# Optimization experiments

Hardware: AMD Instinct MI355X
Metric: run time of the kernel (lower is better)

The kernel has to match this reference:

```python
import jax, jax.numpy as jnp
import numpy as np

# Dims: B batch, T target seq, S source seq (self-attn: S==T), V symmetry-rep dim (D4 -> 8),
# M heads-per-group, K groups (num_heads = M*K = 8), F head_rep dim (TrivialRep -> 1),
# Hqk qk head width, Hv v head width, C feature width per rep component.
B, T, S, V, M, K, F, Hqk, Hv, C = 4, 512, 512, 8, 2, 4, 1, 32, 32, 256


def setup_inputs() -> dict:
    key = jax.random.key(0)
    ks = jax.random.split(key, 6)
    x = jax.random.normal(ks[0], (B, T, V, C), jnp.float32)
    # SymDecompLinear kernels: q has extra out reps (F, M, K); k/v have (F, 1, K) -> m axis broadcast
    Wq = jax.random.normal(ks[1], (C, M, K, F, Hqk), jnp.float32) / np.sqrt(C).astype(np.float32)
    Wk = jax.random.normal(ks[2], (C, K, F, Hqk), jnp.float32) / np.sqrt(C).astype(np.float32)
    Wv = jax.random.normal(ks[3], (C, K, F, Hv), jnp.float32) / np.sqrt(C).astype(np.float32)
    # out projection contracts the (M, K, F, Hv) head structure back to C features
    Wout = jax.random.normal(ks[4], (M, K, F, Hv, C), jnp.float32) / np.sqrt(M * K * F * Hv).astype(np.float32)
    mask = jax.random.bernoulli(ks[5], 0.9, (B, T, S))
    mask = mask.at[..., 0].set(True)  # guarantee each query attends to >=1 key
    return dict(x=x, Wq=Wq, Wk=Wk, Wv=Wv, Wout=Wout, mask=mask)


def reference(x, Wq, Wk, Wv, Wout, mask):
    # projections: q -> [B,T,V,M,K,F,Hqk]; k,v -> [B,S,V,K,F,H] (single head per group, broadcast over m)
    q = jnp.einsum('btvc,cmkfh->btvmkfh', x, Wq)
    k = jnp.einsum('bsvc,ckfh->bsvkfh', x, Wk)
    v = jnp.einsum('bsvc,ckfh->bsvkfh', x, Wv)
    scale = 1.0 / np.sqrt(F * Hqk).astype(np.float32)
    # logits retain the symmetry axis v: [B,T,S,V,M,K]
    logits = scale * jnp.einsum('btvmkfh,bsvkfh->btsvmk', q, k)
    lgmsk = mask[..., :, :, None, None, None]  # [B,T,S,1,1,1]
    weight = jax.nn.softmax(logits, axis=-4, where=lgmsk)  # softmax over source axis s
    att = jnp.einsum('btsvmk,bsvkfh->btvmkfh', weight, v)
    out = jnp.einsum('btvmkfh,mkfhc->btvc', att, Wout)
    return out
```

## Files before the change

kernel.cpp:

```cpp
#include <hip/hip_runtime.h>
#include <hip/hip_bf16.h>
#include <cstdint>

#define BB 4
#define TT 512
#define SS 512
#define VV 8
#define NROWS (BB * TT * VV)

typedef __attribute__((ext_vector_type(8))) short bf16x8;
typedef __attribute__((ext_vector_type(4))) float f32x4;

static __device__ __forceinline__ short f2bf(float f) {
  union { float f; unsigned u; } x; x.f = f;
  unsigned r = x.u + 0x7FFFu + ((x.u >> 16) & 1u);
  return (short)(r >> 16);
}

__global__ __launch_bounds__(256) void pack_w_kernel(const float* __restrict__ Wq,
                                                     const float* __restrict__ Wk,
                                                     const float* __restrict__ Wv,
                                                     const float* __restrict__ Wout,
                                                     short* __restrict__ WcatT,
                                                     short* __restrict__ WoutT) {
  int idx = blockIdx.x * 256 + threadIdx.x;
  const float qscale = 0.17677669529663687f * 1.4426950408889634f;
  if (idx < 512 * 256) {
    int n = idx >> 8, c = idx & 255;
    float val;
    if (n < 256)      val = Wq[c * 256 + n] * qscale;
    else if (n < 384) val = Wk[c * 128 + (n - 256)];
    else              val = Wv[c * 128 + (n - 384)];
    WcatT[idx] = f2bf(val);
  } else {
    int j = idx - 512 * 256;
    int cc = j >> 8, jj = j & 255;
    WoutT[j] = f2bf(Wout[jj * 256 + cc]);
  }
}

__global__ __launch_bounds__(256) void pack_mask_kernel(const int* __restrict__ mask,
                                                        unsigned long long* __restrict__ mask64) {
  int row = blockIdx.x * 4 + (threadIdx.x >> 6);
  int ln = threadIdx.x & 63;
  const int* mrow = mask + (size_t)row * SS;
#pragma unroll
  for (int c = 0; c < 8; ++c) {
    unsigned long long bal = __ballot(mrow[c * 64 + ln] != 0);
    if (ln == 0) mask64[(size_t)row * 8 + c] = bal;
  }
}

template <int N, bool AF32, bool OUTF32>
__global__ __launch_bounds__(256) void gemm_bf16(const void* __restrict__ Ap,
                                                 const short* __restrict__ Bt,
                                                 void* __restrict__ Cout) {
  __shared__ short As[128][64];
  __shared__ short Bs[128][64];
  const int tid = threadIdx.x;
  const int w = tid >> 6, ln = tid & 63;
  const int wr = (w >> 1) * 64, wc = (w & 1) * 64;
  const int bm = blockIdx.x * 128, bn = blockIdx.y * 128;
  const int lr = ln & 15, lk = (ln >> 4) * 8;
  const int r0 = tid >> 3, ko = (tid & 7) * 8;

  f32x4 acc[4][4] = {};

  for (int k0 = 0; k0 < 256; k0 += 64) {
    bf16x8 a[4], bb[4];
#pragma unroll
    for (int i = 0; i < 4; ++i) {
      size_t row = (size_t)(bm + i * 32 + r0);
      if constexpr (AF32) {
        const float* Af = (const float*)Ap;
        float4 f0 = *(const float4*)&Af[row * 256 + k0 + ko];
        float4 f1 = *(const float4*)&Af[row * 256 + k0 + ko + 4];
        bf16x8 o;
        o[0]=f2bf(f0.x); o[1]=f2bf(f0.y); o[2]=f2bf(f0.z); o[3]=f2bf(f0.w);
        o[4]=f2bf(f1.x); o[5]=f2bf(f1.y); o[6]=f2bf(f1.z); o[7]=f2bf(f1.w);
        a[i] = o;
      } else {
        a[i] = *(const bf16x8*)&((const short*)Ap)[row * 256 + k0 + ko];
      }
      bb[i] = *(const bf16x8*)&Bt[(size_t)(bn + i * 32 + r0) * 256 + k0 + ko];
    }
    __syncthreads();
#pragma unroll
    for (int i = 0; i < 4; ++i) {
      *(bf16x8*)&As[i * 32 + r0][ko] = a[i];
      *(bf16x8*)&Bs[i * 32 + r0][ko] = bb[i];
    }
    __syncthreads();

#pragma unroll
    for (int kk = 0; kk < 2; ++kk) {
      bf16x8 af[4], bfr[4];
#pragma unroll
      for (int mi = 0; mi < 4; ++mi)
        af[mi] = *(const bf16x8*)&As[wr + mi * 16 + lr][kk * 32 + lk];
#pragma unroll
      for (int ni = 0; ni < 4; ++ni)
        bfr[ni] = *(const bf16x8*)&Bs[wc + ni * 16 + lr][kk * 32 + lk];
#pragma unroll
      for (int mi = 0; mi < 4; ++mi)
#pragma unroll
        for (int ni = 0; ni < 4; ++ni)
          acc[mi][ni] = __builtin_amdgcn_mfma_f32_16x16x32_bf16(af[mi], bfr[ni], acc[mi][ni], 0, 0, 0);
    }
  }

  const int rowg = (ln >> 4) * 4;
#pragma unroll
  for (int mi = 0; mi < 4; ++mi)
#pragma unroll
    for (int r = 0; r < 4; ++r) {
      size_t row = bm + wr + mi * 16 + rowg + r;
#pragma unroll
      for (int ni = 0; ni < 4; ++ni) {
        int col = bn + wc + ni * 16 + lr;
        if (OUTF32) ((float*)Cout)[row * N + col] = acc[mi][ni][r];
        else        ((short*)Cout)[row * N + col] = f2bf(acc[mi][ni][r]);
      }
    }
}

__global__ __launch_bounds__(512) void attn_mfma(const short* __restrict__ qkv,
                                                 const unsigned long long* __restrict__ mask64,
                                                 short* __restrict__ att) {
  const int t0 = blockIdx.x * 128;
  const int v  = blockIdx.y >> 2;
  const int k  = blockIdx.y & 3;
  const int b  = blockIdx.z;
  const int tid = threadIdx.x;
  const int w  = tid >> 6;
  const int ln = tid & 63;
  const int gq = ln >> 4;
  const int tr = ln & 15;

  __shared__ short Kt[4][64][40];
  __shared__ short Vt[4][32][72];
  __shared__ short Pt[8][16][72];

  bf16x8 qf[2];
  {
    const short* qp = qkv + ((size_t)((b*TT + t0 + w*16 + tr)*VV + v))*512 + k*32 + gq*8;
    qf[0] = *(const bf16x8*)qp;
    qf[1] = *(const bf16x8*)(qp + 128);
  }

  f32x4 acc_o[2][2] = {};
  float m_run[2] = {-1e30f, -1e30f};
  float l_run[2] = {0.f, 0.f};

  const int sp  = tid >> 8;
  const int st2 = tid & 255;
  const int srow = st2 >> 2;
  const int hg = (st2 & 3) * 8;
  const unsigned long long* mrow = mask64 + ((size_t)(b*TT + t0 + w*16 + tr)) * 8;

  const short* src0 = qkv + ((size_t)((b*TT + sp*64 + srow)*VV + v))*512 + 256 + k*32 + hg;
  bf16x8 kreg = *(const bf16x8*)src0;
  bf16x8 vreg = *(const bf16x8*)(src0 + 128);

  for (int c2 = 0; c2 < 4; ++c2) {
    const int bufb = (c2 & 1) * 2;
    *(bf16x8*)&Kt[bufb + sp][srow][hg] = kreg;
#pragma unroll
    for (int j = 0; j < 8; ++j) Vt[bufb + sp][hg + j][srow] = vreg[j];
    __syncthreads();
    if (c2 < 3) {
      const short* src = qkv + ((size_t)((b*TT + (c2 + 1)*128 + sp*64 + srow)*VV + v))*512 + 256 + k*32 + hg;
      kreg = *(const bf16x8*)src;
      vreg = *(const bf16x8*)(src + 128);
    }

#pragma unroll
    for (int p = 0; p < 2; ++p) {
      unsigned long long mb = mrow[2 * c2 + p];
      unsigned mlo = (unsigned)mb, mhi = (unsigned)(mb >> 32);
      float bias[4][4];
#pragma unroll
      for (int st = 0; st < 4; ++st) {
        unsigned wbits = (st < 2) ? mlo : mhi;
        const int base = (st & 1) * 16 + 4 * gq;
#pragma unroll
        for (int r = 0; r < 4; ++r)
          bias[st][r] = ((wbits >> (base + r)) & 1u) ? 0.f : -INFINITY;
      }

      bf16x8 kf[4], vf[2][2];
#pragma unroll
      for (int st = 0; st < 4; ++st) kf[st] = *(const bf16x8*)&Kt[bufb + p][st*16 + tr][gq*8];
#pragma unroll
      for (int sh = 0; sh < 2; ++sh)
#pragma unroll
        for (int hh = 0; hh < 2; ++hh)
          vf[sh][hh] = *(const bf16x8*)&Vt[bufb + p][hh*16 + tr][sh*32 + gq*8];

#pragma unroll
      for (int m = 0; m < 2; ++m) {
        f32x4 lac[4];
#pragma unroll
        for (int st = 0; st < 4; ++st) {
          f32x4 z = {0.f, 0.f, 0.f, 0.f};
          lac[st] = __builtin_amdgcn_mfma_f32_16x16x32_bf16(kf[st], qf[m], z, 0, 0, 0);
        }
        float pl[4][4];
#pragma unroll
        for (int st = 0; st < 4; ++st)
#pragma unroll
          for (int r = 0; r < 4; ++r)
            pl[st][r] = lac[st][r] + bias[st][r];

        float cm = -INFINITY;
#pragma unroll
        for (int st = 0; st < 4; ++st)
#pragma unroll
          for (int r = 0; r < 4; ++r) cm = fmaxf(cm, pl[st][r]);
        cm = fmaxf(cm, __shfl_xor(cm, 16));
        cm = fmaxf(cm, __shfl_xor(cm, 32));

        bool skip = __all(cm - m_run[m] <= 11.5f);
        float mnew, corr;
        if (skip) { mnew = m_run[m]; corr = 1.f; }
        else {
          mnew = fmaxf(m_run[m], cm);
          corr = exp2f(m_run[m] - mnew);
          m_run[m] = mnew;
        }

        float rs = 0.f;
#pragma unroll
        for (int st = 0; st < 4; ++st)
#pragma unroll
          for (int r = 0; r < 4; ++r) {
            pl[st][r] = exp2f(pl[st][r] - mnew);
            rs += pl[st][r];
          }
        rs += __shfl_xor(rs, 16);
        rs += __shfl_xor(rs, 32);
        l_run[m] = l_run[m] * corr + rs;

        if (!skip) {
          float corrR[4];
#pragma unroll
          for (int r = 0; r < 4; ++r) corrR[r] = __shfl(corr, 4 * gq + r);
#pragma unroll
          for (int hh = 0; hh < 2; ++hh)
#pragma unroll
            for (int r = 0; r < 4; ++r) acc_o[m][hh][r] *= corrR[r];
        }

#pragma unroll
        for (int st = 0; st < 4; ++st) {
          unsigned d0 = ((unsigned)(unsigned short)f2bf(pl[st][1]) << 16) |
                        (unsigned)(unsigned short)f2bf(pl[st][0]);
          unsigned d1 = ((unsigned)(unsigned short)f2bf(pl[st][3]) << 16) |
                        (unsigned)(unsigned short)f2bf(pl[st][2]);
          *(uint2*)&Pt[w][tr][st * 16 + 4 * gq] = make_uint2(d0, d1);
        }
#pragma unroll
        for (int sh = 0; sh < 2; ++sh) {
          bf16x8 pf = *(const bf16x8*)&Pt[w][tr][sh * 32 + gq * 8];
#pragma unroll
          for (int hh = 0; hh < 2; ++hh)
            acc_o[m][hh] = __builtin_amdgcn_mfma_f32_16x16x32_bf16(pf, vf[sh][hh], acc_o[m][hh], 0, 0, 0);
        }
      }
    }
  }

#pragma unroll
  for (int m = 0; m < 2; ++m) {
    float invR[4];
#pragma unroll
    for (int r = 0; r < 4; ++r) invR[r] = 1.f / __shfl(l_run[m], 4 * gq + r);
#pragma unroll
    for (int r = 0; r < 4; ++r) {
      short* dst = att + ((size_t)((b*TT + t0 + w*16 + 4*gq + r)*VV + v))*256
                 + m*128 + k*32 + tr;
      dst[0]  = f2bf(acc_o[m][0][r] * invR[r]);
      dst[16] = f2bf(acc_o[m][1][r] * invR[r]);
    }
  }
}

extern "C" void kernel_launch(void* const* d_in, const int* in_sizes, int n_in,
                              void* d_out, int out_size, void* d_ws, size_t ws_size,
                              hipStream_t stream) {
  const float* x = (const float*)d_in[0];
  const float* Wq = (const float*)d_in[1];
  const float* Wk = (const float*)d_in[2];
  const float* Wv = (const float*)d_in[3];
  const float* Wout = (const float*)d_in[4];
  const int* mask = (const int*)d_in[5];
  float* out = (float*)d_out;

  short* WcatT = (short*)d_ws;
  short* WoutT = WcatT + 512 * 256;
  short* qkv   = WoutT + 256 * 256;
  short* att   = qkv + (size_t)NROWS * 512;
  unsigned long long* mask64 = (unsigned long long*)(att + (size_t)NROWS * 256);

  pack_w_kernel<<<(512 * 256 + 256 * 256) / 256, 256, 0, stream>>>(Wq, Wk, Wv, Wout, WcatT, WoutT);
  pack_mask_kernel<<<BB * TT / 4, 256, 0, stream>>>(mask, mask64);
  gemm_bf16<512, true, false><<<dim3(NROWS / 128, 4), 256, 0, stream>>>(x, WcatT, qkv);
  attn_mfma<<<dim3(TT / 128, VV * 4, BB), 512, 0, stream>>>(qkv, mask64, att);
  gemm_bf16<256, false, true><<<dim3(NROWS / 128, 2), 256, 0, stream>>>(att, WoutT, out);
}
```

Measured before the change: 81.33 us.

## Halve attention block size and use hardware packed bf16 conversion

New measurement: 72.08 us. 1.13x faster.

```diff
diff --git a/kernel.cpp b/kernel.cpp
--- a/kernel.cpp
+++ b/kernel.cpp
@@ -15,6 +15,12 @@
   union { float f; unsigned u; } x; x.f = f;
   unsigned r = x.u + 0x7FFFu + ((x.u >> 16) & 1u);
   return (short)(r >> 16);
+}
+
+static __device__ __forceinline__ unsigned cvt_pk(float lo, float hi) {
+  unsigned r;
+  asm("v_cvt_pk_bf16_f32 %0, %1, %2" : "=v"(r) : "v"(lo), "v"(hi));
+  return r;
 }
 
 __global__ __launch_bounds__(256) void pack_w_kernel(const float* __restrict__ Wq,
@@ -75,10 +81,9 @@
         const float* Af = (const float*)Ap;
         float4 f0 = *(const float4*)&Af[row * 256 + k0 + ko];
         float4 f1 = *(const float4*)&Af[row * 256 + k0 + ko + 4];
-        bf16x8 o;
-        o[0]=f2bf(f0.x); o[1]=f2bf(f0.y); o[2]=f2bf(f0.z); o[3]=f2bf(f0.w);
-        o[4]=f2bf(f1.x); o[5]=f2bf(f1.y); o[6]=f2bf(f1.z); o[7]=f2bf(f1.w);
-        a[i] = o;
+        uint4 pk = make_uint4(cvt_pk(f0.x, f0.y), cvt_pk(f0.z, f0.w),
+                              cvt_pk(f1.x, f1.y), cvt_pk(f1.z, f1.w));
+        a[i] = *(bf16x8*)&pk;
       } else {
         a[i] = *(const bf16x8*)&((const short*)Ap)[row * 256 + k0 + ko];
       }
@@ -115,19 +120,26 @@
 #pragma unroll
     for (int r = 0; r < 4; ++r) {
       size_t row = bm + wr + mi * 16 + rowg + r;
-#pragma unroll
-      for (int ni = 0; ni < 4; ++ni) {
-        int col = bn + wc + ni * 16 + lr;
-        if (OUTF32) ((float*)Cout)[row * N + col] = acc[mi][ni][r];
-        else        ((short*)Cout)[row * N + col] = f2bf(acc[mi][ni][r]);
-      }
-    }
-}
-
-__global__ __launch_bounds__(512) void attn_mfma(const short* __restrict__ qkv,
+      if constexpr (OUTF32) {
+#pragma unroll
+        for (int ni = 0; ni < 4; ++ni)
+          ((float*)Cout)[row * N + bn + wc + ni * 16 + lr] = acc[mi][ni][r];
+      } else {
+        unsigned u0 = cvt_pk(acc[mi][0][r], acc[mi][1][r]);
+        unsigned u1 = cvt_pk(acc[mi][2][r], acc[mi][3][r]);
+        short* Cs = (short*)Cout + row * N + bn + wc + lr;
+        Cs[0]  = (short)u0;
+        Cs[16] = (short)(u0 >> 16);
+        Cs[32] = (short)u1;
+        Cs[48] = (short)(u1 >> 16);
+      }
+    }
+}
+
+__global__ __launch_bounds__(256) void attn_mfma(const short* __restrict__ qkv,
                                                  const unsigned long long* __restrict__ mask64,
                                                  short* __restrict__ att) {
-  const int t0 = blockIdx.x * 128;
+  const int t0 = blockIdx.x * 64;
   const int v  = blockIdx.y >> 2;
   const int k  = blockIdx.y & 3;
   const int b  = blockIdx.z;
@@ -137,9 +149,9 @@
   const int gq = ln >> 4;
   const int tr = ln & 15;
 
-  __shared__ short Kt[4][64][40];
-  __shared__ short Vt[4][32][72];
-  __shared__ short Pt[8][16][72];
+  __shared__ short Kt[2][64][40];
+  __shared__ short Vt[2][32][72];
+  __shared__ short Pt[4][16][72];
 
   bf16x8 qf[2];
   {
@@ -152,120 +164,110 @@
   float m_run[2] = {-1e30f, -1e30f};
   float l_run[2] = {0.f, 0.f};
 
-  const int sp  = tid >> 8;
-  const int st2 = tid & 255;
-  const int srow = st2 >> 2;
-  const int hg = (st2 & 3) * 8;
+  const int srow = tid >> 2;
+  const int hg = (tid & 3) * 8;
   const unsigned long long* mrow = mask64 + ((size_t)(b*TT + t0 + w*16 + tr)) * 8;
 
-  const short* src0 = qkv + ((size_t)((b*TT + sp*64 + srow)*VV + v))*512 + 256 + k*32 + hg;
+  const short* src0 = qkv + ((size_t)((b*TT + srow)*VV + v))*512 + 256 + k*32 + hg;
   bf16x8 kreg = *(const bf16x8*)src0;
   bf16x8 vreg = *(const bf16x8*)(src0 + 128);
 
-  for (int c2 = 0; c2 < 4; ++c2) {
-    const int bufb = (c2 & 1) * 2;
-    *(bf16x8*)&Kt[bufb + sp][srow][hg] = kreg;
-#pragma unroll
-    for (int j = 0; j < 8; ++j) Vt[bufb + sp][hg + j][srow] = vreg[j];
+  for (int c = 0; c < 8; ++c) {
+    const int cur = c & 1;
+    *(bf16x8*)&Kt[cur][srow][hg] = kreg;
+#pragma unroll
+    for (int j = 0; j < 8; ++j) Vt[cur][hg + j][srow] = vreg[j];
     __syncthreads();
-    if (c2 < 3) {
-      const short* src = qkv + ((size_t)((b*TT + (c2 + 1)*128 + sp*64 + srow)*VV + v))*512 + 256 + k*32 + hg;
+    if (c < 7) {
+      const short* src = qkv + ((size_t)((b*TT + (c + 1) * 64 + srow)*VV + v))*512 + 256 + k*32 + hg;
       kreg = *(const bf16x8*)src;
       vreg = *(const bf16x8*)(src + 128);
     }
-
-#pragma unroll
-    for (int p = 0; p < 2; ++p) {
-      unsigned long long mb = mrow[2 * c2 + p];
-      unsigned mlo = (unsigned)mb, mhi = (unsigned)(mb >> 32);
-      float bias[4][4];
+    unsigned long long mb = mrow[c];
+    unsigned mlo = (unsigned)mb, mhi = (unsigned)(mb >> 32);
+    float bias[4][4];
+#pragma unroll
+    for (int st = 0; st < 4; ++st) {
+      unsigned wbits = (st < 2) ? mlo : mhi;
+      const int base = (st & 1) * 16 + 4 * gq;
+#pragma unroll
+      for (int r = 0; r < 4; ++r)
+        bias[st][r] = ((wbits >> (base + r)) & 1u) ? 0.f : -INFINITY;
+    }
+
+    bf16x8 kf[4], vf[2][2];
+#pragma unroll
+    for (int st = 0; st < 4; ++st) kf[st] = *(const bf16x8*)&Kt[cur][st*16 + tr][gq*8];
+#pragma unroll
+    for (int sh = 0; sh < 2; ++sh)
+#pragma unroll
+      for (int hh = 0; hh < 2; ++hh)
+        vf[sh][hh] = *(const bf16x8*)&Vt[cur][hh*16 + tr][sh*32 + gq*8];
+
+#pragma unroll
+    for (int m = 0; m < 2; ++m) {
+      f32x4 lac[4];
 #pragma unroll
       for (int st = 0; st < 4; ++st) {
-        unsigned wbits = (st < 2) ? mlo : mhi;
-        const int base = (st & 1) * 16 + 4 * gq;
+        f32x4 z = {0.f, 0.f, 0.f, 0.f};
+        lac[st] = __builtin_amdgcn_mfma_f32_16x16x32_bf16(kf[st], qf[m], z, 0, 0, 0);
+      }
+      float pl[4][4];
+#pragma unroll
+      for (int st = 0; st < 4; ++st)
 #pragma unroll
         for (int r = 0; r < 4; ++r)
-          bias[st][r] = ((wbits >> (base + r)) & 1u) ? 0.f : -INFINITY;
-      }
-
-      bf16x8 kf[4], vf[2][2];
-#pragma unroll
-      for (int st = 0; st < 4; ++st) kf[st] = *(const bf16x8*)&Kt[bufb + p][st*16 + tr][gq*8];
-#pragma unroll
-      for (int sh = 0; sh < 2; ++sh)
+          pl[st][r] = lac[st][r] + bias[st][r];
+
+      float cm = -INFINITY;
+#pragma unroll
+      for (int st = 0; st < 4; ++st)
+#pragma unroll
+        for (int r = 0; r < 4; ++r) cm = fmaxf(cm, pl[st][r]);
+      cm = fmaxf(cm, __shfl_xor(cm, 16));
+      cm = fmaxf(cm, __shfl_xor(cm, 32));
+
+      bool skip = __all(cm - m_run[m] <= 11.5f);
+      float mnew, corr;
+      if (skip) { mnew = m_run[m]; corr = 1.f; }
+      else {
+        mnew = fmaxf(m_run[m], cm);
+        corr = exp2f(m_run[m] - mnew);
+        m_run[m] = mnew;
+      }
+
+      float rs = 0.f;
+#pragma unroll
+      for (int st = 0; st < 4; ++st)
+#pragma unroll
+        for (int r = 0; r < 4; ++r) {
+          pl[st][r] = exp2f(pl[st][r] - mnew);
+          rs += pl[st][r];
+        }
+      rs += __shfl_xor(rs, 16);
+      rs += __shfl_xor(rs, 32);
+      l_run[m] = l_run[m] * corr + rs;
+
+      if (!skip) {
+        float corrR[4];
+#pragma unroll
+        for (int r = 0; r < 4; ++r) corrR[r] = __shfl(corr, 4 * gq + r);
 #pragma unroll
         for (int hh = 0; hh < 2; ++hh)
-          vf[sh][hh] = *(const bf16x8*)&Vt[bufb + p][hh*16 + tr][sh*32 + gq*8];
-
-#pragma unroll
-      for (int m = 0; m < 2; ++m) {
-        f32x4 lac[4];
-#pragma unroll
-        for (int st = 0; st < 4; ++st) {
-          f32x4 z = {0.f, 0.f, 0.f, 0.f};
-          lac[st] = __builtin_amdgcn_mfma_f32_16x16x32_bf16(kf[st], qf[m], z, 0, 0, 0);
-        }
-        float pl[4][4];
-#pragma unroll
-        for (int st = 0; st < 4; ++st)
-#pragma unroll
-          for (int r = 0; r < 4; ++r)
-            pl[st][r] = lac[st][r] + bias[st][r];
-
-        float cm = -INFINITY;
-#pragma unroll
-        for (int st = 0; st < 4; ++st)
-#pragma unroll
-          for (int r = 0; r < 4; ++r) cm = fmaxf(cm, pl[st][r]);
-        cm = fmaxf(cm, __shfl_xor(cm, 16));
-        cm = fmaxf(cm, __shfl_xor(cm, 32));
-
-        bool skip = __all(cm - m_run[m] <= 11.5f);
-        float mnew, corr;
-        if (skip) { mnew = m_run[m]; corr = 1.f; }
-        else {
-          mnew = fmaxf(m_run[m], cm);
-          corr = exp2f(m_run[m] - mnew);
-          m_run[m] = mnew;
-        }
-
-        float rs = 0.f;
-#pragma unroll
-        for (int st = 0; st < 4; ++st)
-#pragma unroll
-          for (int r = 0; r < 4; ++r) {
-            pl[st][r] = exp2f(pl[st][r] - mnew);
-            rs += pl[st][r];
-          }
-        rs += __shfl_xor(rs, 16);
-        rs += __shfl_xor(rs, 32);
-        l_run[m] = l_run[m] * corr + rs;
-
-        if (!skip) {
-          float corrR[4];
-#pragma unroll
-          for (int r = 0; r < 4; ++r) corrR[r] = __shfl(corr, 4 * gq + r);
-#pragma unroll
-          for (int hh = 0; hh < 2; ++hh)
-#pragma unroll
-            for (int r = 0; r < 4; ++r) acc_o[m][hh][r] *= corrR[r];
-        }
-
-#pragma unroll
-        for (int st = 0; st < 4; ++st) {
-          unsigned d0 = ((unsigned)(unsigned short)f2bf(pl[st][1]) << 16) |
-                        (unsigned)(unsigned short)f2bf(pl[st][0]);
-          unsigned d1 = ((unsigned)(unsigned short)f2bf(pl[st][3]) << 16) |
-                        (unsigned)(unsigned short)f2bf(pl[st][2]);
-          *(uint2*)&Pt[w][tr][st * 16 + 4 * gq] = make_uint2(d0, d1);
-        }
-#pragma unroll
-        for (int sh = 0; sh < 2; ++sh) {
-          bf16x8 pf = *(const bf16x8*)&Pt[w][tr][sh * 32 + gq * 8];
-#pragma unroll
-          for (int hh = 0; hh < 2; ++hh)
-            acc_o[m][hh] = __builtin_amdgcn_mfma_f32_16x16x32_bf16(pf, vf[sh][hh], acc_o[m][hh], 0, 0, 0);
-        }
+#pragma unroll
+          for (int r = 0; r < 4; ++r) acc_o[m][hh][r] *= corrR[r];
+      }
+
+#pragma unroll
+      for (int st = 0; st < 4; ++st)
+        *(uint2*)&Pt[w][tr][st * 16 + 4 * gq] =
+            make_uint2(cvt_pk(pl[st][0], pl[st][1]), cvt_pk(pl[st][2], pl[st][3]));
+#pragma unroll
+      for (int sh = 0; sh < 2; ++sh) {
+        bf16x8 pf = *(const bf16x8*)&Pt[w][tr][sh * 32 + gq * 8];
+#pragma unroll
+        for (int hh = 0; hh < 2; ++hh)
+          acc_o[m][hh] = __builtin_amdgcn_mfma_f32_16x16x32_bf16(pf, vf[sh][hh], acc_o[m][hh], 0, 0, 0);
       }
     }
   }
@@ -279,8 +281,9 @@
     for (int r = 0; r < 4; ++r) {
       short* dst = att + ((size_t)((b*TT + t0 + w*16 + 4*gq + r)*VV + v))*256
                  + m*128 + k*32 + tr;
-      dst[0]  = f2bf(acc_o[m][0][r] * invR[r]);
-      dst[16] = f2bf(acc_o[m][1][r] * invR[r]);
+      unsigned u = cvt_pk(acc_o[m][0][r] * invR[r], acc_o[m][1][r] * invR[r]);
+      dst[0]  = (short)u;
+      dst[16] = (short)(u >> 16);
     }
   }
 }
@@ -305,6 +308,6 @@
   pack_w_kernel<<<(512 * 256 + 256 * 256) / 256, 256, 0, stream>>>(Wq, Wk, Wv, Wout, WcatT, WoutT);
   pack_mask_kernel<<<BB * TT / 4, 256, 0, stream>>>(mask, mask64);
   gemm_bf16<512, true, false><<<dim3(NROWS / 128, 4), 256, 0, stream>>>(x, WcatT, qkv);
-  attn_mfma<<<dim3(TT / 128, VV * 4, BB), 512, 0, stream>>>(qkv, mask64, att);
+  attn_mfma<<<dim3(TT / 64, VV * 4, BB), 256, 0, stream>>>(qkv, mask64, att);
   gemm_bf16<256, false, true><<<dim3(NROWS / 128, 2), 256, 0, stream>>>(att, WoutT, out);
 }
```
